# Performance work log

Measured on AMD Instinct MI355X. Metric: run time of the kernel, lower is better.

Reference implementation:

```python
import jax, jax.numpy as jnp
import numpy as np

EPS = 1e-6


def setup_inputs() -> dict:
    key = jax.random.key(0)
    kx, ky = jax.random.split(key)
    B, C, H, W = 8, 128, 48, 64
    x = jax.random.normal(kx, (B, C, H, W), dtype=jnp.float32)
    y = jax.random.normal(ky, (B, C, H, W), dtype=jnp.float32)
    return {"x": x, "y": y}


def reference(x, y):
    # x, y: (b, c, h, w)
    b, c, h, w = x.shape
    # torch: x.transpose(2,3).view(b,c,h*w) -> x flattened w-major,
    #        so output channel k = v*h + u corresponds to x[:, :, u, v].
    # corr5[b, v, u, i, j] = sum_c x[b,c,u,v] * y[b,c,i,j]
    corr = jnp.einsum('bcuv,bcij->bvuij', x, y)
    corr = corr.reshape(b, w * h, h, w)  # channel k = v*h + u
    # normalization: ReLU then L2-normalize over the h*w channel dim
    corr = jax.nn.relu(corr)
    norm = jnp.sqrt(jnp.sum(corr * corr, axis=1, keepdims=True) + EPS)
    return corr / norm
```

## Files before the change

### kernel.cpp

```cpp
#include <hip/hip_runtime.h>
#include <hip/hip_bf16.h>

#define NB 8
#define NC 128
#define NH 48
#define NW 64
#define NS 3072
#define EPSF 1e-6f

#define GLOBAL_AS __attribute__((address_space(1)))
#define LDS_AS __attribute__((address_space(3)))

typedef __bf16 bf16x8 __attribute__((ext_vector_type(8)));
typedef float f32x4 __attribute__((ext_vector_type(4)));

__device__ __forceinline__ unsigned short bf16_rtne(float f) {
  union { float f; unsigned u; } c;
  c.f = f;
  unsigned r = (c.u + 0x7fffu + ((c.u >> 16) & 1u)) >> 16;
  return (unsigned short)r;
}

__global__ __launch_bounds__(256) void transpose_both(
    const float* __restrict__ x, const float* __restrict__ y,
    __hip_bfloat16* __restrict__ AT, __hip_bfloat16* __restrict__ BT) {
  __shared__ float tile[32 * 129];
  const int id = blockIdx.x;
  const int b = id & 7;
  const int which = (id >> 3) & 1;
  const int f0 = (id >> 4) * 32;
  const float* src = which ? y : x;
  __hip_bfloat16* dst = which ? BT : AT;
  const int t = threadIdx.x;

  {
    const int fl = (t & 7) * 4, cg0 = t >> 3;
    const float* sp = src + (size_t)b * NC * NS + f0 + fl;
#pragma unroll
    for (int i = 0; i < 4; ++i) {
      int cg = cg0 + i * 32;
      f32x4 v = *(const f32x4*)(sp + (size_t)cg * NS);
      tile[(fl + 0) * 129 + cg] = v[0];
      tile[(fl + 1) * 129 + cg] = v[1];
      tile[(fl + 2) * 129 + cg] = v[2];
      tile[(fl + 3) * 129 + cg] = v[3];
    }
  }
  __syncthreads();
  {
    const int c4 = (t & 31) * 4, kl0 = t >> 5;
    unsigned short* dp = (unsigned short*)dst;
#pragma unroll
    for (int i = 0; i < 4; ++i) {
      int fl = kl0 + i * 8;
      int f = f0 + fl;
      int k = which ? f : ((f & 63) * NH + (f >> 6));
      f32x4 v = *(const f32x4*)&tile[fl * 129 + c4];
      ushort4 u4;
      u4.x = bf16_rtne(v[0]);
      u4.y = bf16_rtne(v[1]);
      u4.z = bf16_rtne(v[2]);
      u4.w = bf16_rtne(v[3]);
      *(ushort4*)(dp + ((size_t)b * NS + k) * NC + c4) = u4;
    }
  }
}

template <int CPW>
__device__ __forceinline__ void stage_tile(const char* gsrc, char* ldst,
                                           int wid, int lane) {
  const int lr = lane >> 4, lg = lane & 15;
#pragma unroll
  for (int i = 0; i < CPW; ++i) {
    int c = wid * CPW + i;
    int row = c * 4 + lr;
    int g = lg ^ (row & 7);
    __builtin_amdgcn_global_load_lds(
        (const GLOBAL_AS unsigned*)(gsrc + row * 256 + g * 16),
        (LDS_AS unsigned*)(ldst + c * 1024), 16, 0, 0);
  }
}

__device__ __forceinline__ void gemm_acc(const char* As, const char* Bs,
                                         float cs[2], int wm, int wn, int l15,
                                         int kg) {
  f32x4 acc[4][2] = {};
  const int rx = l15 & 7;
#pragma unroll
  for (int kk = 0; kk < 4; ++kk) {
    int g = (kk * 4 + kg) ^ rx;
    bf16x8 a[4], bb[2];
#pragma unroll
    for (int mi = 0; mi < 4; ++mi)
      a[mi] = *(const bf16x8*)(As + (wm * 64 + mi * 16 + l15) * 256 + g * 16);
#pragma unroll
    for (int ni = 0; ni < 2; ++ni)
      bb[ni] = *(const bf16x8*)(Bs + (wn * 32 + ni * 16 + l15) * 256 + g * 16);
#pragma unroll
    for (int mi = 0; mi < 4; ++mi)
#pragma unroll
      for (int ni = 0; ni < 2; ++ni)
        acc[mi][ni] = __builtin_amdgcn_mfma_f32_16x16x32_bf16(
            a[mi], bb[ni], acc[mi][ni], 0, 0, 0);
  }
#pragma unroll
  for (int ni = 0; ni < 2; ++ni)
#pragma unroll
    for (int mi = 0; mi < 4; ++mi)
#pragma unroll
      for (int r = 0; r < 4; ++r) {
        float v = fmaxf(acc[mi][ni][r], 0.f);
        cs[ni] += v * v;
      }
}

__global__ __launch_bounds__(512, 1) void corr_part_p(
    const __hip_bfloat16* __restrict__ AT,
    const __hip_bfloat16* __restrict__ BT, float* __restrict__ part) {
  __shared__ char smem[98304];
  char* Bs = smem + 65536;
  const int id = blockIdx.x;
  const int b = id & 7;
  const int tl = id >> 3;
  const int nt = tl >> 2, mq = tl & 3;
  const int t = threadIdx.x;
  const int lane = t & 63, wid = t >> 6;
  const int wm = wid >> 2, wn = wid & 3;
  const int l15 = lane & 15, kg = lane >> 4;

  const char* Ab = (const char*)(AT + ((size_t)b * NS + mq * 768) * NC);
  const char* Bg = (const char*)(BT + ((size_t)b * NS + nt * 128) * NC);

  stage_tile<4>(Bg, Bs, wid, lane);
  stage_tile<4>(Ab, smem, wid, lane);
  asm volatile("s_waitcnt vmcnt(0)" ::: "memory");
  __builtin_amdgcn_sched_barrier(0);
  __builtin_amdgcn_s_barrier();

  float cs[2] = {0.f, 0.f};
  int cur = 0;
#pragma unroll 1
  for (int i = 0; i < 6; ++i) {
    if (i + 1 < 6)
      stage_tile<4>(Ab + (size_t)(i + 1) * 32768, smem + ((cur ^ 1) * 32768),
                    wid, lane);
    gemm_acc(smem + cur * 32768, Bs, cs, wm, wn, l15, kg);
    asm volatile("s_waitcnt vmcnt(0)" ::: "memory");
    __builtin_amdgcn_sched_barrier(0);
    __builtin_amdgcn_s_barrier();
    cur ^= 1;
  }

#pragma unroll
  for (int ni = 0; ni < 2; ++ni) {
    cs[ni] += __shfl_xor(cs[ni], 16, 64);
    cs[ni] += __shfl_xor(cs[ni], 32, 64);
  }
  float* csum = (float*)smem;
  if (kg == 0) {
#pragma unroll
    for (int ni = 0; ni < 2; ++ni)
      csum[wm * 128 + wn * 32 + ni * 16 + l15] = cs[ni];
  }
  __syncthreads();
  if (t < 128) {
    float s = csum[t] + csum[128 + t];
    part[(size_t)mq * (NB * NS) + (size_t)b * NS + nt * 128 + t] = s;
  }
}

__global__ __launch_bounds__(256, 2) void corr_out(
    const __hip_bfloat16* __restrict__ AT,
    const __hip_bfloat16* __restrict__ BT, const float* __restrict__ part_in,
    float* __restrict__ out) {
  __shared__ char smem[66560];
  float* rnc = (float*)(smem + 65536);
  const int id = blockIdx.x;
  const int b = id & 7;
  const int tl = id >> 3;
  const int mt = tl / 24, nt = tl - mt * 24;
  const int t = threadIdx.x;
  const int lane = t & 63, wid = t >> 6;
  const int wm = wid >> 1, wn = wid & 1;
  const int l15 = lane & 15, kg = lane >> 4;

  const char* Ag = (const char*)(AT + ((size_t)b * NS + mt * 128) * NC);
  const char* Bg = (const char*)(BT + ((size_t)b * NS + nt * 128) * NC);
  stage_tile<8>(Ag, smem, wid, lane);
  stage_tile<8>(Bg, smem + 32768, wid, lane);
  if (t < 128) {
    float s = 0.f;
#pragma unroll
    for (int q = 0; q < 4; ++q)
      s += part_in[(size_t)q * (NB * NS) + (size_t)b * NS + nt * 128 + t];
    rnc[t] = rsqrtf(s + EPSF);
  }
  __syncthreads();

  f32x4 acc[4][4] = {};
  const int rx = l15 & 7;
#pragma unroll
  for (int kk = 0; kk < 4; ++kk) {
    int g = (kk * 4 + kg) ^ rx;
    bf16x8 a[4], bb[4];
#pragma unroll
    for (int mi = 0; mi < 4; ++mi)
      a[mi] = *(const bf16x8*)(smem + (wm * 64 + mi * 16 + l15) * 256 + g * 16);
#pragma unroll
    for (int ni = 0; ni < 4; ++ni)
      bb[ni] = *(const bf16x8*)(smem + 32768 +
                                (wn * 64 + ni * 16 + l15) * 256 + g * 16);
#pragma unroll
    for (int mi = 0; mi < 4; ++mi)
#pragma unroll
      for (int ni = 0; ni < 4; ++ni)
        acc[mi][ni] = __builtin_amdgcn_mfma_f32_16x16x32_bf16(
            a[mi], bb[ni], acc[mi][ni], 0, 0, 0);
  }

  float rnv[4];
#pragma unroll
  for (int ni = 0; ni < 4; ++ni) rnv[ni] = rnc[wn * 64 + ni * 16 + l15];
  __syncthreads();

  float* tf = (float*)smem;
#pragma unroll
  for (int mi = 0; mi < 4; ++mi)
#pragma unroll
    for (int ni = 0; ni < 4; ++ni)
#pragma unroll
      for (int r = 0; r < 4; ++r) {
        int row = wm * 64 + mi * 16 + kg * 4 + r;
        int col = wn * 64 + ni * 16 + l15;
        tf[row * 129 + col] = fmaxf(acc[mi][ni][r], 0.f) * rnv[ni];
      }
  __syncthreads();

  float* ob = out + (size_t)b * NS * NS + (size_t)(mt * 128) * NS + nt * 128;
  const int rsub = t >> 5, c4 = (t & 31) * 4;
#pragma unroll
  for (int it = 0; it < 16; ++it) {
    int row = it * 8 + rsub;
    f32x4 v = *(const f32x4*)&tf[row * 129 + c4];
    __builtin_nontemporal_store(v, (f32x4*)&ob[(size_t)row * NS + c4]);
  }
}

extern "C" void kernel_launch(void* const* d_in, const int* in_sizes, int n_in,
                              void* d_out, int out_size, void* d_ws,
                              size_t ws_size, hipStream_t stream) {
  const float* x = (const float*)d_in[0];
  const float* y = (const float*)d_in[1];
  float* out = (float*)d_out;
  char* ws = (char*)d_ws;

  const size_t AT_OFF = 0;
  const size_t BT_OFF = 6291456;
  const size_t PART_OFF = 12582912;
  const size_t NEED = 12976128;
  if (ws_size < NEED) return;

  __hip_bfloat16* AT = (__hip_bfloat16*)(ws + AT_OFF);
  __hip_bfloat16* BT = (__hip_bfloat16*)(ws + BT_OFF);
  float* part = (float*)(ws + PART_OFF);

  transpose_both<<<dim3(1536), dim3(256), 0, stream>>>(x, y, AT, BT);
  corr_part_p<<<dim3(768), dim3(512), 0, stream>>>(AT, BT, part);
  corr_out<<<dim3(4608), dim3(256), 0, stream>>>(AT, BT, part, out);
}
```

Before: 95.21 us.

## Split column-norm pass into more smaller blocks with single-buffered A tiles

Restructures the column sum-of-squares kernel so that 1536 blocks of 256 threads each cover 384 rows, replacing 768 blocks of 512 threads that each covered 768 rows. The goal is higher occupancy: two blocks per CU on 64KB of shared memory, with a 64x64 tile per warp. The A tile is now single-buffered and loaded synchronously each iteration, so the previous prefetch overlap is lost. The partial-sum buffer grows to 8 slices, and the output kernel reduces 8 partials.

```diff
diff --git a/kernel.cpp b/kernel.cpp
--- a/kernel.cpp
+++ b/kernel.cpp
@@ -81,91 +81,82 @@
   }
 }
 
-__device__ __forceinline__ void gemm_acc(const char* As, const char* Bs,
-                                         float cs[2], int wm, int wn, int l15,
-                                         int kg) {
-  f32x4 acc[4][2] = {};
-  const int rx = l15 & 7;
-#pragma unroll
-  for (int kk = 0; kk < 4; ++kk) {
-    int g = (kk * 4 + kg) ^ rx;
-    bf16x8 a[4], bb[2];
-#pragma unroll
-    for (int mi = 0; mi < 4; ++mi)
-      a[mi] = *(const bf16x8*)(As + (wm * 64 + mi * 16 + l15) * 256 + g * 16);
-#pragma unroll
-    for (int ni = 0; ni < 2; ++ni)
-      bb[ni] = *(const bf16x8*)(Bs + (wn * 32 + ni * 16 + l15) * 256 + g * 16);
-#pragma unroll
-    for (int mi = 0; mi < 4; ++mi)
-#pragma unroll
-      for (int ni = 0; ni < 2; ++ni)
-        acc[mi][ni] = __builtin_amdgcn_mfma_f32_16x16x32_bf16(
-            a[mi], bb[ni], acc[mi][ni], 0, 0, 0);
-  }
-#pragma unroll
-  for (int ni = 0; ni < 2; ++ni)
-#pragma unroll
-    for (int mi = 0; mi < 4; ++mi)
-#pragma unroll
-      for (int r = 0; r < 4; ++r) {
-        float v = fmaxf(acc[mi][ni][r], 0.f);
-        cs[ni] += v * v;
-      }
-}
-
-__global__ __launch_bounds__(512, 1) void corr_part_p(
+__global__ __launch_bounds__(256, 2) void corr_part_v2(
     const __hip_bfloat16* __restrict__ AT,
     const __hip_bfloat16* __restrict__ BT, float* __restrict__ part) {
-  __shared__ char smem[98304];
-  char* Bs = smem + 65536;
+  __shared__ char smem[65536];
+  char* As = smem;
+  char* Bs = smem + 32768;
   const int id = blockIdx.x;
   const int b = id & 7;
   const int tl = id >> 3;
-  const int nt = tl >> 2, mq = tl & 3;
+  const int nt = tl >> 3;
+  const int mg = tl & 7;
   const int t = threadIdx.x;
   const int lane = t & 63, wid = t >> 6;
-  const int wm = wid >> 2, wn = wid & 3;
+  const int wm = wid >> 1, wn = wid & 1;
   const int l15 = lane & 15, kg = lane >> 4;
 
-  const char* Ab = (const char*)(AT + ((size_t)b * NS + mq * 768) * NC);
+  const char* Ab = (const char*)(AT + ((size_t)b * NS + mg * 384) * NC);
   const char* Bg = (const char*)(BT + ((size_t)b * NS + nt * 128) * NC);
 
-  stage_tile<4>(Bg, Bs, wid, lane);
-  stage_tile<4>(Ab, smem, wid, lane);
-  asm volatile("s_waitcnt vmcnt(0)" ::: "memory");
-  __builtin_amdgcn_sched_barrier(0);
-  __builtin_amdgcn_s_barrier();
-
-  float cs[2] = {0.f, 0.f};
-  int cur = 0;
+  stage_tile<8>(Bg, Bs, wid, lane);
+
+  float cs[4] = {0.f, 0.f, 0.f, 0.f};
+  const int rx = l15 & 7;
 #pragma unroll 1
-  for (int i = 0; i < 6; ++i) {
-    if (i + 1 < 6)
-      stage_tile<4>(Ab + (size_t)(i + 1) * 32768, smem + ((cur ^ 1) * 32768),
-                    wid, lane);
-    gemm_acc(smem + cur * 32768, Bs, cs, wm, wn, l15, kg);
+  for (int i = 0; i < 3; ++i) {
+    stage_tile<8>(Ab + (size_t)i * 32768, As, wid, lane);
     asm volatile("s_waitcnt vmcnt(0)" ::: "memory");
     __builtin_amdgcn_sched_barrier(0);
     __builtin_amdgcn_s_barrier();
-    cur ^= 1;
-  }
-
-#pragma unroll
-  for (int ni = 0; ni < 2; ++ni) {
+
+    f32x4 acc[4][4] = {};
+#pragma unroll
+    for (int kk = 0; kk < 4; ++kk) {
+      int g = (kk * 4 + kg) ^ rx;
+      bf16x8 a[4], bb[4];
+#pragma unroll
+      for (int mi = 0; mi < 4; ++mi)
+        a[mi] = *(const bf16x8*)(As + (wm * 64 + mi * 16 + l15) * 256 + g * 16);
+#pragma unroll
+      for (int ni = 0; ni < 4; ++ni)
+        bb[ni] =
+            *(const bf16x8*)(Bs + (wn * 64 + ni * 16 + l15) * 256 + g * 16);
+#pragma unroll
+      for (int mi = 0; mi < 4; ++mi)
+#pragma unroll
+        for (int ni = 0; ni < 4; ++ni)
+          acc[mi][ni] = __builtin_amdgcn_mfma_f32_16x16x32_bf16(
+              a[mi], bb[ni], acc[mi][ni], 0, 0, 0);
+    }
+#pragma unroll
+    for (int ni = 0; ni < 4; ++ni)
+#pragma unroll
+      for (int mi = 0; mi < 4; ++mi)
+#pragma unroll
+        for (int r = 0; r < 4; ++r) {
+          float v = fmaxf(acc[mi][ni][r], 0.f);
+          cs[ni] += v * v;
+        }
+    __builtin_amdgcn_s_barrier();
+  }
+
+#pragma unroll
+  for (int ni = 0; ni < 4; ++ni) {
     cs[ni] += __shfl_xor(cs[ni], 16, 64);
     cs[ni] += __shfl_xor(cs[ni], 32, 64);
   }
   float* csum = (float*)smem;
   if (kg == 0) {
 #pragma unroll
-    for (int ni = 0; ni < 2; ++ni)
-      csum[wm * 128 + wn * 32 + ni * 16 + l15] = cs[ni];
+    for (int ni = 0; ni < 4; ++ni)
+      csum[wm * 128 + wn * 64 + ni * 16 + l15] = cs[ni];
   }
   __syncthreads();
   if (t < 128) {
     float s = csum[t] + csum[128 + t];
-    part[(size_t)mq * (NB * NS) + (size_t)b * NS + nt * 128 + t] = s;
+    part[(size_t)mg * (NB * NS) + (size_t)b * NS + nt * 128 + t] = s;
   }
 }
 
@@ -191,7 +182,7 @@
   if (t < 128) {
     float s = 0.f;
 #pragma unroll
-    for (int q = 0; q < 4; ++q)
+    for (int q = 0; q < 8; ++q)
       s += part_in[(size_t)q * (NB * NS) + (size_t)b * NS + nt * 128 + t];
     rnc[t] = rsqrtf(s + EPSF);
   }
@@ -257,7 +248,7 @@
   const size_t AT_OFF = 0;
   const size_t BT_OFF = 6291456;
   const size_t PART_OFF = 12582912;
-  const size_t NEED = 12976128;
+  const size_t NEED = 13369344;
   if (ws_size < NEED) return;
 
   __hip_bfloat16* AT = (__hip_bfloat16*)(ws + AT_OFF);
@@ -265,6 +256,6 @@
   float* part = (float*)(ws + PART_OFF);
 
   transpose_both<<<dim3(1536), dim3(256), 0, stream>>>(x, y, AT, BT);
-  corr_part_p<<<dim3(768), dim3(512), 0, stream>>>(AT, BT, part);
+  corr_part_v2<<<dim3(1536), dim3(256), 0, stream>>>(AT, BT, part);
   corr_out<<<dim3(4608), dim3(256), 0, stream>>>(AT, BT, part, out);
 }
```

After: 90.80 us. 1.05x faster.
